# Kernel optimization log

Hardware: AMD Instinct MI355X
Metric: run time of the kernel (lower is better)

## Reference

```python
import jax, jax.numpy as jnp
import numpy as np

ALPHA = 0.25
GAMMA = 2.0
MARGIN = 1.0
LAMBDA_GRAPH = 0.1
N = 8192
D = 128


def setup_inputs() -> dict:
    key = jax.random.key(0)
    k1, k2, k3, k4 = jax.random.split(key, 4)
    preds = jax.random.normal(k1, (N,), dtype=jnp.float32)
    targets = jax.random.randint(k2, (N,), 0, 2).astype(jnp.float32)  # binary labels
    features = jax.random.normal(k3, (N, D), dtype=jnp.float32)
    graph_features = jax.random.normal(k4, (N, D), dtype=jnp.float32)
    return {"preds": preds, "targets": targets, "features": features,
            "graph_features": graph_features}


def _focal_loss(preds, targets):
    # numerically stable BCE-with-logits, reduction='none'
    bce = jnp.maximum(preds, 0.0) - preds * targets + jnp.log1p(jnp.exp(-jnp.abs(preds)))
    pt = jnp.exp(-bce)
    return jnp.mean(ALPHA * (1.0 - pt) ** GAMMA * bce)


def _contrastive_loss(features, labels):
    # squared pairwise distances via ||a||^2 + ||b||^2 - 2 a.b  -> [N, N]
    sqn = jnp.sum(features * features, axis=-1)
    sq = sqn[:, None] + sqn[None, :] - 2.0 * (features @ features.T)
    sq = jnp.maximum(sq, 0.0)
    # safe sqrt (gradient-safe at 0)
    pos = sq > 0.0
    dist = jnp.where(pos, jnp.sqrt(jnp.where(pos, sq, 1.0)), 0.0)
    same = labels[:, None] == labels[None, :]
    # same-label pairs: dist^2 == sq ; different: clamp(margin - dist, 0)^2
    per_pair = jnp.where(same, sq, jnp.maximum(MARGIN - dist, 0.0) ** 2)
    return jnp.mean(per_pair)  # sum / N^2


def _graph_reg_loss(graph_features):
    diff = graph_features[1:] - graph_features[:-1]
    return jnp.mean(jnp.sqrt(jnp.sum(diff * diff, axis=1)))


def reference(preds, targets, features, graph_features):
    return (_focal_loss(preds, targets)
            + _contrastive_loss(features, targets)
            + LAMBDA_GRAPH * _graph_reg_loss(graph_features))
```

## Files before the change

### kernel.cpp

```cpp
#include <hip/hip_runtime.h>
#include <hip/hip_bf16.h>


#define N_PTS 8192
#define DIM 128

typedef __bf16 bf16x8 __attribute__((ext_vector_type(8)));
typedef float f32x4 __attribute__((ext_vector_type(4)));

#define FBF_OFF   0
#define SQN_OFF   2097152
#define CPART_OFF 2129920
#define FPART_OFF 2163200
#define GPART_OFF 2163328
#define VPART_OFF 2164352
#define ASCR_OFF  2197120
#define BSCR_OFF  2721408

__global__ __launch_bounds__(256) void aux_kernel(const float* __restrict__ feat,
                                                  const float* __restrict__ preds,
                                                  const float* __restrict__ targets,
                                                  const float* __restrict__ gfeat,
                                                  __bf16* __restrict__ fbf,
                                                  __bf16* __restrict__ ascr,
                                                  __bf16* __restrict__ bscr,
                                                  float* __restrict__ sqn,
                                                  float* __restrict__ vpart,
                                                  float* __restrict__ f_part,
                                                  float* __restrict__ g_part) {
    __shared__ __align__(16) char smem[8192];
    const int bx = blockIdx.x;
    const int tid = threadIdx.x;
    const int w = tid >> 6;
    const int lane = tid & 63;

    if (bx < 512) {
        const int g = bx;
        const float4* feat4 = reinterpret_cast<const float4*>(feat);
        const float4 a = feat4[g * 512 + tid * 2];
        const float4 b = feat4[g * 512 + tid * 2 + 1];
        const int m = tid >> 4, c = tid & 15;
        union { __bf16 h[8]; uint4 u; } pk;
        pk.h[0] = (__bf16)a.x; pk.h[1] = (__bf16)a.y;
        pk.h[2] = (__bf16)a.z; pk.h[3] = (__bf16)a.w;
        pk.h[4] = (__bf16)b.x; pk.h[5] = (__bf16)b.y;
        pk.h[6] = (__bf16)b.z; pk.h[7] = (__bf16)b.w;
        *reinterpret_cast<uint4*>(smem + c * 256 + m * 16) = pk.u;
        if (c < 3) {
            union { __bf16 h[8]; uint4 u; } pa;
            pa.h[0] = (__bf16)(-2.f * a.x); pa.h[1] = (__bf16)(-2.f * a.y);
            pa.h[2] = (__bf16)(-2.f * a.z); pa.h[3] = (__bf16)(-2.f * a.w);
            pa.h[4] = (__bf16)(-2.f * b.x); pa.h[5] = (__bf16)(-2.f * b.y);
            pa.h[6] = (__bf16)(-2.f * b.z); pa.h[7] = (__bf16)(-2.f * b.w);
            *reinterpret_cast<uint4*>(smem + 4096 + c * 256 + m * 16) = pa.u;
            *reinterpret_cast<uint4*>(smem + 5120 + c * 256 + m * 16) = pk.u;
        }
        const float s = a.x * a.x + a.y * a.y + a.z * a.z + a.w * a.w
                      + b.x * b.x + b.y * b.y + b.z * b.z + b.w * b.w;
        reinterpret_cast<float*>(smem + 6144)[m * 16 + c] = s;
        __syncthreads();
        if (c == 3) {
            const float* S = reinterpret_cast<const float*>(smem + 6144);
            const float sq24 = S[m * 16] + S[m * 16 + 1] + S[m * 16 + 2];
            union { __bf16 h[8]; uint4 u; } pa, pb;
            #pragma unroll
            for (int k = 0; k < 8; ++k) { pa.h[k] = (__bf16)0.f; pb.h[k] = (__bf16)0.f; }
            pa.h[0] = (__bf16)sq24; pa.h[1] = (__bf16)1.f;
            pb.h[0] = (__bf16)1.f;  pb.h[1] = (__bf16)sq24;
            *reinterpret_cast<uint4*>(smem + 4096 + 3 * 256 + m * 16) = pa.u;
            *reinterpret_cast<uint4*>(smem + 5120 + 3 * 256 + m * 16) = pb.u;
        }
        if (c == 0) {
            const float* S = reinterpret_cast<const float*>(smem + 6144);
            float t = 0.f;
            #pragma unroll
            for (int k = 0; k < 16; ++k) t += S[m * 16 + k];
            sqn[g * 16 + m] = t;
        }
        __syncthreads();
        reinterpret_cast<uint4*>(fbf)[g * 256 + tid] =
            *reinterpret_cast<const uint4*>(smem + tid * 16);
        if (tid < 64)
            reinterpret_cast<uint4*>(ascr)[g * 64 + tid] =
                *reinterpret_cast<const uint4*>(smem + 4096 + tid * 16);
        else if (tid < 128)
            reinterpret_cast<uint4*>(bscr)[g * 64 + (tid - 64)] =
                *reinterpret_cast<const uint4*>(smem + 5120 + (tid - 64) * 16);
    } else if (bx < 544) {
        const int b = bx - 512;
        const float2* feat2 = reinterpret_cast<const float2*>(feat);
        float2 accA = {0.f, 0.f}, acc1 = {0.f, 0.f};
        int r = b * 256 + w * 64;
        #pragma unroll 4
        for (int i = 0; i < 64; ++i, ++r) {
            const float2 v = feat2[r * 64 + lane];
            const float tr = targets[r];
            accA.x += v.x; accA.y += v.y;
            acc1.x += tr * v.x; acc1.y += tr * v.y;
        }
        float* fA = reinterpret_cast<float*>(smem);
        float* f1 = reinterpret_cast<float*>(smem + 2048);
        fA[w * 128 + 2 * lane] = accA.x; fA[w * 128 + 2 * lane + 1] = accA.y;
        f1[w * 128 + 2 * lane] = acc1.x; f1[w * 128 + 2 * lane + 1] = acc1.y;
        __syncthreads();
        if (tid < 128) {
            const int d = tid;
            const float c1 = f1[d] + f1[128 + d] + f1[256 + d] + f1[384 + d];
            const float ca = fA[d] + fA[128 + d] + fA[256 + d] + fA[384 + d];
            vpart[b * 256 + tid] = ca - c1;
        } else {
            const int d = tid - 128;
            vpart[b * 256 + tid] = f1[d] + f1[128 + d] + f1[256 + d] + f1[384 + d];
        }
    } else if (bx < 576) {
        const int b = bx - 544;
        const int i = b * 256 + tid;
        const float p = preds[i], t = targets[i];
        const float bce = fmaxf(p, 0.f) - p * t + log1pf(expf(-fabsf(p)));
        const float pt = expf(-bce);
        const float om = 1.f - pt;
        float v = 0.25f * om * om * bce;
        #pragma unroll
        for (int off = 32; off > 0; off >>= 1) v += __shfl_down(v, off);
        float* red = reinterpret_cast<float*>(smem);
        if (lane == 0) red[w] = v;
        __syncthreads();
        if (tid == 0) f_part[b] = red[0] + red[1] + red[2] + red[3];
    } else {
        const int b = bx - 576;
        float acc = 0.f;
        #pragma unroll
        for (int it = 0; it < 8; ++it) {
            const int r = b * 4 + w + it * 1024;
            if (r < N_PTS - 1) {
                const float2 a = *reinterpret_cast<const float2*>(gfeat + r * DIM + lane * 2);
                const float2 bb = *reinterpret_cast<const float2*>(gfeat + (r + 1) * DIM + lane * 2);
                const float dx = bb.x - a.x, dy = bb.y - a.y;
                float s = dx * dx + dy * dy;
                #pragma unroll
                for (int off = 32; off > 0; off >>= 1) s += __shfl_down(s, off);
                if (lane == 0) acc += sqrtf(s);
            }
        }
        float* red = reinterpret_cast<float*>(smem);
        if (lane == 0) red[w] = acc;
        __syncthreads();
        if (tid == 0) g_part[b] = red[0] + red[1] + red[2] + red[3];
    }
}

template<bool DIAG>
__device__ __forceinline__ float scan_slow(const f32x4 (&acc)[4][4],
                                           const f32x4 (&sqni)[4], const f32x4 (&ti4)[4],
                                           const float (&sqnj)[4], const float (&tj4)[4],
                                           int wm, int wn, int quad, int m15) {
    float lsum = 0.f;
    #pragma unroll
    for (int tm = 0; tm < 4; ++tm) {
        #pragma unroll
        for (int tn = 0; tn < 4; ++tn) {
            const int jl = wn * 64 + tn * 16 + m15;
            #pragma unroll
            for (int e = 0; e < 4; ++e) {
                const float sq = sqni[tm][e] + sqnj[tn] - 2.f * acc[tm][tn][e];
                bool excl = (ti4[tm][e] == tj4[tn]);
                if (DIAG) {
                    const int il = wm * 64 + tm * 16 + quad * 4 + e;
                    excl = excl || (jl <= il);
                }
                if (!excl && sq < 1.f) {
                    const float d = sqrtf(fmaxf(sq, 0.f));
                    const float m = 1.f - d;
                    lsum += 2.f * m * m;
                }
            }
        }
    }
    return lsum;
}

__global__ __launch_bounds__(256, 4) void pair_kernel(const __bf16* __restrict__ fbf,
                                                      const __bf16* __restrict__ ascr,
                                                      const __bf16* __restrict__ bscr,
                                                      const float* __restrict__ sqn,
                                                      const float* __restrict__ targets,
                                                      float* __restrict__ c_part) {
    const int u = blockIdx.x;
    const int v = 2079 - u;
    int k = (int)((sqrtf(8.f * (float)v + 1.f) - 1.f) * 0.5f);
    while ((k + 1) * (k + 2) / 2 <= v) ++k;
    while (k * (k + 1) / 2 > v) --k;
    const int bi = 63 - k;
    const int bj = 63 - (v - k * (k + 1) / 2);

    const int tid = threadIdx.x;
    const int lane = tid & 63;
    const int wv = tid >> 6;
    const int quad = lane >> 4;
    const int m15 = lane & 15;
    const int wm = wv >> 1, wn = wv & 1;
    const int ibase = bi * 128, jbase = bj * 128;

    const uint4* aS = reinterpret_cast<const uint4*>(ascr);
    const uint4* bS = reinterpret_cast<const uint4*>(bscr);
    const int gA = bi * 8 + wm * 4, gB = bj * 8 + wn * 4;
    bf16x8 afs[4], bfs[4];
    #pragma unroll
    for (int t = 0; t < 4; ++t) {
        afs[t] = *reinterpret_cast<const bf16x8*>(aS + (gA + t) * 64 + quad * 16 + m15);
        bfs[t] = *reinterpret_cast<const bf16x8*>(bS + (gB + t) * 64 + quad * 16 + m15);
    }
    f32x4 acc[4][4];
    #pragma unroll
    for (int a = 0; a < 4; ++a)
        #pragma unroll
        for (int b = 0; b < 4; ++b) acc[a][b] = (f32x4){0.f, 0.f, 0.f, 0.f};
    #pragma unroll
    for (int tm = 0; tm < 4; ++tm)
        #pragma unroll
        for (int tn = 0; tn < 4; ++tn)
            acc[tm][tn] = __builtin_amdgcn_mfma_f32_16x16x32_bf16(
                afs[tm], bfs[tn], acc[tm][tn], 0, 0, 0);

    float minl = 1e30f;
    #pragma unroll
    for (int tm = 0; tm < 4; ++tm)
        #pragma unroll
        for (int tn = 0; tn < 4; ++tn)
            #pragma unroll
            for (int e = 0; e < 4; ++e)
                minl = fminf(minl, acc[tm][tn][e]);

    float lsum = 0.f;
    if (__any(minl < 2.f)) {
        f32x4 sqni[4], ti4[4];
        float sqnj[4], tj4[4];
        #pragma unroll
        for (int tm = 0; tm < 4; ++tm) {
            const int i0 = wm * 64 + tm * 16 + quad * 4;
            sqni[tm] = *reinterpret_cast<const f32x4*>(sqn + ibase + i0);
            ti4[tm]  = *reinterpret_cast<const f32x4*>(targets + ibase + i0);
        }
        #pragma unroll
        for (int tn = 0; tn < 4; ++tn) {
            const int jl = wn * 64 + tn * 16 + m15;
            sqnj[tn] = sqn[jbase + jl];
            tj4[tn]  = targets[jbase + jl];
        }
        #pragma unroll
        for (int a = 0; a < 4; ++a)
            #pragma unroll
            for (int b = 0; b < 4; ++b) acc[a][b] = (f32x4){0.f, 0.f, 0.f, 0.f};
        const uint4* fp = reinterpret_cast<const uint4*>(fbf);
        const uint4* base_a = fp + (bi * 8 + wm * 4) * 256 + quad * 16 + m15;
        const uint4* base_b = fp + (bj * 8 + wn * 4) * 256 + quad * 16 + m15;
        #pragma unroll
        for (int ks = 0; ks < 4; ++ks) {
            bf16x8 af[4], bfr[4];
            #pragma unroll
            for (int t = 0; t < 4; ++t) {
                af[t]  = *reinterpret_cast<const bf16x8*>(base_a + t * 256 + ks * 64);
                bfr[t] = *reinterpret_cast<const bf16x8*>(base_b + t * 256 + ks * 64);
            }
            #pragma unroll
            for (int tm = 0; tm < 4; ++tm)
                #pragma unroll
                for (int tn = 0; tn < 4; ++tn)
                    acc[tm][tn] = __builtin_amdgcn_mfma_f32_16x16x32_bf16(
                        af[tm], bfr[tn], acc[tm][tn], 0, 0, 0);
        }
        lsum = (bi == bj)
            ? scan_slow<true >(acc, sqni, ti4, sqnj, tj4, wm, wn, quad, m15)
            : scan_slow<false>(acc, sqni, ti4, sqnj, tj4, wm, wn, quad, m15);
        #pragma unroll
        for (int off = 32; off > 0; off >>= 1) lsum += __shfl_down(lsum, off);
    }
    if (lane == 0) c_part[u * 4 + wv] = lsum;
}

__global__ __launch_bounds__(256) void finalize_kernel(const float* __restrict__ c_part,
                                                       const float* __restrict__ f_part,
                                                       const float* __restrict__ g_part,
                                                       const float* __restrict__ vpart,
                                                       const float* __restrict__ sqn,
                                                       const float* __restrict__ targets,
                                                       float* __restrict__ out) {
    __shared__ float red[32];
    const int tid = threadIdx.x;
    const int w = tid >> 6, lane = tid & 63;

    float c = 0.f;
    for (int i = tid; i < 8320; i += 256) c += c_part[i];
    float f = (tid < 32) ? f_part[tid] : 0.f;
    float g = g_part[tid];

    float V = 0.f;
    #pragma unroll 8
    for (int b = 0; b < 32; ++b) V += vpart[b * 256 + tid];
    float vsq = V * V;

    float stot = 0.f, s1 = 0.f, n1 = 0.f;
    for (int i = tid; i < N_PTS; i += 256) {
        const float s = sqn[i], t = targets[i];
        stot += s; s1 += t * s; n1 += t;
    }

    #pragma unroll
    for (int off = 32; off > 0; off >>= 1) {
        c += __shfl_down(c, off);
        f += __shfl_down(f, off);
        g += __shfl_down(g, off);
        vsq  += __shfl_down(vsq, off);
        stot += __shfl_down(stot, off);
        s1   += __shfl_down(s1, off);
        n1   += __shfl_down(n1, off);
    }
    if (lane == 0) {
        red[w] = c; red[4 + w] = f; red[8 + w] = g;
        red[12 + w] = vsq; red[16 + w] = stot; red[20 + w] = s1; red[24 + w] = n1;
    }
    __syncthreads();
    if (tid == 0) {
        const double cs = (double)red[0] + red[1] + red[2] + red[3];
        const double fs = (double)red[4] + red[5] + red[6] + red[7];
        const double gs = (double)red[8] + red[9] + red[10] + red[11];
        const double v0sq = (double)red[12] + red[13];
        const double v1sq = (double)red[14] + red[15];
        const double st = (double)red[16] + red[17] + red[18] + red[19];
        const double s1s = (double)red[20] + red[21] + red[22] + red[23];
        const double n1s = (double)red[24] + red[25] + red[26] + red[27];
        const double n0s = (double)N_PTS - n1s;
        const double s0s = st - s1s;
        const double same = 2.0 * (n0s * s0s - v0sq) + 2.0 * (n1s * s1s - v1sq);
        out[0] = (float)((cs + same) / ((double)N_PTS * N_PTS)
                         + fs / N_PTS + 0.1 * (gs / (N_PTS - 1)));
    }
}

extern "C" void kernel_launch(void* const* d_in, const int* in_sizes, int n_in,
                              void* d_out, int out_size, void* d_ws, size_t ws_size,
                              hipStream_t stream) {
    const float* preds    = (const float*)d_in[0];
    const float* targets  = (const float*)d_in[1];
    const float* features = (const float*)d_in[2];
    const float* gfeat    = (const float*)d_in[3];
    char* ws = (char*)d_ws;
    __bf16* fbf   = (__bf16*)(ws + FBF_OFF);
    __bf16* ascr  = (__bf16*)(ws + ASCR_OFF);
    __bf16* bscr  = (__bf16*)(ws + BSCR_OFF);
    float* sqn    = (float*)(ws + SQN_OFF);
    float* c_part = (float*)(ws + CPART_OFF);
    float* f_part = (float*)(ws + FPART_OFF);
    float* g_part = (float*)(ws + GPART_OFF);
    float* vpart  = (float*)(ws + VPART_OFF);
    float* out = (float*)d_out;

    aux_kernel<<<832, 256, 0, stream>>>(features, preds, targets, gfeat,
                                        fbf, ascr, bscr, sqn, vpart, f_part, g_part);
    pair_kernel<<<2080, 256, 0, stream>>>(fbf, ascr, bscr, sqn, targets, c_part);
    finalize_kernel<<<1, 256, 0, stream>>>(c_part, f_part, g_part, vpart, sqn, targets, out);
}
```

Baseline: 102.4 us.

## Fuse bf16 conversion into pair kernel and replace finalize with atomic last-block reduction

Drops the bf16 pre-conversion pass and its scratch buffers. The pair blocks now load fp32 features directly, convert them to bf16 in registers and compute squared norms on the fly. The separate finalize kernel is replaced by double-precision atomic accumulators plus a block counter, so the last finishing block writes the output. The launch count drops from three to two, at the cost of redundant fp32 loads and conversions in each pair tile, plus atomic contention.

```diff
diff --git a/kernel.cpp b/kernel.cpp
--- a/kernel.cpp
+++ b/kernel.cpp
@@ -8,144 +8,82 @@
 typedef __bf16 bf16x8 __attribute__((ext_vector_type(8)));
 typedef float f32x4 __attribute__((ext_vector_type(4)));
 
-#define FBF_OFF   0
-#define SQN_OFF   2097152
-#define CPART_OFF 2129920
-#define FPART_OFF 2163200
-#define GPART_OFF 2163328
-#define VPART_OFF 2164352
-#define ASCR_OFF  2197120
-#define BSCR_OFF  2721408
-
-__global__ __launch_bounds__(256) void aux_kernel(const float* __restrict__ feat,
-                                                  const float* __restrict__ preds,
-                                                  const float* __restrict__ targets,
-                                                  const float* __restrict__ gfeat,
-                                                  __bf16* __restrict__ fbf,
-                                                  __bf16* __restrict__ ascr,
-                                                  __bf16* __restrict__ bscr,
-                                                  float* __restrict__ sqn,
-                                                  float* __restrict__ vpart,
-                                                  float* __restrict__ f_part,
-                                                  float* __restrict__ g_part) {
-    __shared__ __align__(16) char smem[8192];
-    const int bx = blockIdx.x;
+#define VPART_OFF 0
+#define SPART_OFF (128 * 256 * 4)
+#define CTRL_OFF  (SPART_OFF + 128 * 16)
+
+#define NPAIR 2080
+#define NFOCAL 32
+#define NGRAPH 256
+#define TOTAL_BLOCKS (NPAIR + NFOCAL + NGRAPH + 1)
+
+__device__ __forceinline__ bf16x8 pack8(const float4 a, const float4 b) {
+    bf16x8 r;
+    r[0] = (__bf16)a.x; r[1] = (__bf16)a.y; r[2] = (__bf16)a.z; r[3] = (__bf16)a.w;
+    r[4] = (__bf16)b.x; r[5] = (__bf16)b.y; r[6] = (__bf16)b.z; r[7] = (__bf16)b.w;
+    return r;
+}
+__device__ __forceinline__ float ssq8(const float4 a, const float4 b) {
+    return a.x * a.x + a.y * a.y + a.z * a.z + a.w * a.w
+         + b.x * b.x + b.y * b.y + b.z * b.z + b.w * b.w;
+}
+
+__global__ __launch_bounds__(256) void prep_kernel(const float* __restrict__ feat,
+                                                   const float* __restrict__ targets,
+                                                   float* __restrict__ vpart,
+                                                   float* __restrict__ spart,
+                                                   unsigned long long* __restrict__ ctrl) {
+    const int b = blockIdx.x;
     const int tid = threadIdx.x;
-    const int w = tid >> 6;
-    const int lane = tid & 63;
-
-    if (bx < 512) {
-        const int g = bx;
-        const float4* feat4 = reinterpret_cast<const float4*>(feat);
-        const float4 a = feat4[g * 512 + tid * 2];
-        const float4 b = feat4[g * 512 + tid * 2 + 1];
-        const int m = tid >> 4, c = tid & 15;
-        union { __bf16 h[8]; uint4 u; } pk;
-        pk.h[0] = (__bf16)a.x; pk.h[1] = (__bf16)a.y;
-        pk.h[2] = (__bf16)a.z; pk.h[3] = (__bf16)a.w;
-        pk.h[4] = (__bf16)b.x; pk.h[5] = (__bf16)b.y;
-        pk.h[6] = (__bf16)b.z; pk.h[7] = (__bf16)b.w;
-        *reinterpret_cast<uint4*>(smem + c * 256 + m * 16) = pk.u;
-        if (c < 3) {
-            union { __bf16 h[8]; uint4 u; } pa;
-            pa.h[0] = (__bf16)(-2.f * a.x); pa.h[1] = (__bf16)(-2.f * a.y);
-            pa.h[2] = (__bf16)(-2.f * a.z); pa.h[3] = (__bf16)(-2.f * a.w);
-            pa.h[4] = (__bf16)(-2.f * b.x); pa.h[5] = (__bf16)(-2.f * b.y);
-            pa.h[6] = (__bf16)(-2.f * b.z); pa.h[7] = (__bf16)(-2.f * b.w);
-            *reinterpret_cast<uint4*>(smem + 4096 + c * 256 + m * 16) = pa.u;
-            *reinterpret_cast<uint4*>(smem + 5120 + c * 256 + m * 16) = pk.u;
-        }
-        const float s = a.x * a.x + a.y * a.y + a.z * a.z + a.w * a.w
-                      + b.x * b.x + b.y * b.y + b.z * b.z + b.w * b.w;
-        reinterpret_cast<float*>(smem + 6144)[m * 16 + c] = s;
-        __syncthreads();
-        if (c == 3) {
-            const float* S = reinterpret_cast<const float*>(smem + 6144);
-            const float sq24 = S[m * 16] + S[m * 16 + 1] + S[m * 16 + 2];
-            union { __bf16 h[8]; uint4 u; } pa, pb;
-            #pragma unroll
-            for (int k = 0; k < 8; ++k) { pa.h[k] = (__bf16)0.f; pb.h[k] = (__bf16)0.f; }
-            pa.h[0] = (__bf16)sq24; pa.h[1] = (__bf16)1.f;
-            pb.h[0] = (__bf16)1.f;  pb.h[1] = (__bf16)sq24;
-            *reinterpret_cast<uint4*>(smem + 4096 + 3 * 256 + m * 16) = pa.u;
-            *reinterpret_cast<uint4*>(smem + 5120 + 3 * 256 + m * 16) = pb.u;
-        }
-        if (c == 0) {
-            const float* S = reinterpret_cast<const float*>(smem + 6144);
-            float t = 0.f;
-            #pragma unroll
-            for (int k = 0; k < 16; ++k) t += S[m * 16 + k];
-            sqn[g * 16 + m] = t;
-        }
-        __syncthreads();
-        reinterpret_cast<uint4*>(fbf)[g * 256 + tid] =
-            *reinterpret_cast<const uint4*>(smem + tid * 16);
-        if (tid < 64)
-            reinterpret_cast<uint4*>(ascr)[g * 64 + tid] =
-                *reinterpret_cast<const uint4*>(smem + 4096 + tid * 16);
-        else if (tid < 128)
-            reinterpret_cast<uint4*>(bscr)[g * 64 + (tid - 64)] =
-                *reinterpret_cast<const uint4*>(smem + 5120 + (tid - 64) * 16);
-    } else if (bx < 544) {
-        const int b = bx - 512;
-        const float2* feat2 = reinterpret_cast<const float2*>(feat);
-        float2 accA = {0.f, 0.f}, acc1 = {0.f, 0.f};
-        int r = b * 256 + w * 64;
-        #pragma unroll 4
-        for (int i = 0; i < 64; ++i, ++r) {
-            const float2 v = feat2[r * 64 + lane];
-            const float tr = targets[r];
-            accA.x += v.x; accA.y += v.y;
-            acc1.x += tr * v.x; acc1.y += tr * v.y;
-        }
-        float* fA = reinterpret_cast<float*>(smem);
-        float* f1 = reinterpret_cast<float*>(smem + 2048);
-        fA[w * 128 + 2 * lane] = accA.x; fA[w * 128 + 2 * lane + 1] = accA.y;
-        f1[w * 128 + 2 * lane] = acc1.x; f1[w * 128 + 2 * lane + 1] = acc1.y;
-        __syncthreads();
-        if (tid < 128) {
-            const int d = tid;
-            const float c1 = f1[d] + f1[128 + d] + f1[256 + d] + f1[384 + d];
-            const float ca = fA[d] + fA[128 + d] + fA[256 + d] + fA[384 + d];
-            vpart[b * 256 + tid] = ca - c1;
-        } else {
-            const int d = tid - 128;
-            vpart[b * 256 + tid] = f1[d] + f1[128 + d] + f1[256 + d] + f1[384 + d];
-        }
-    } else if (bx < 576) {
-        const int b = bx - 544;
-        const int i = b * 256 + tid;
-        const float p = preds[i], t = targets[i];
-        const float bce = fmaxf(p, 0.f) - p * t + log1pf(expf(-fabsf(p)));
-        const float pt = expf(-bce);
-        const float om = 1.f - pt;
-        float v = 0.25f * om * om * bce;
-        #pragma unroll
-        for (int off = 32; off > 0; off >>= 1) v += __shfl_down(v, off);
-        float* red = reinterpret_cast<float*>(smem);
-        if (lane == 0) red[w] = v;
-        __syncthreads();
-        if (tid == 0) f_part[b] = red[0] + red[1] + red[2] + red[3];
+    if (b == 128) {
+        if (tid == 0) {
+            *reinterpret_cast<unsigned*>(ctrl) = 0u;
+            double* a = reinterpret_cast<double*>(ctrl);
+            a[1] = 0.0; a[2] = 0.0; a[3] = 0.0;
+        }
+        return;
+    }
+    __shared__ float fA[512], f1[512];
+    __shared__ float sred[4][3];
+    const int w = tid >> 6, lane = tid & 63;
+    const float2* feat2 = reinterpret_cast<const float2*>(feat);
+    float2 accA = {0.f, 0.f}, acc1 = {0.f, 0.f};
+    float ssqA = 0.f, ssq1 = 0.f, n1 = 0.f;
+    int r = b * 64 + w * 16;
+    #pragma unroll 4
+    for (int i = 0; i < 16; ++i, ++r) {
+        const float2 v = feat2[r * 64 + lane];
+        const float tr = targets[r];
+        accA.x += v.x; accA.y += v.y;
+        acc1.x += tr * v.x; acc1.y += tr * v.y;
+        const float s2 = v.x * v.x + v.y * v.y;
+        ssqA += s2; ssq1 += tr * s2; n1 += tr;
+    }
+    fA[w * 128 + 2 * lane] = accA.x; fA[w * 128 + 2 * lane + 1] = accA.y;
+    f1[w * 128 + 2 * lane] = acc1.x; f1[w * 128 + 2 * lane + 1] = acc1.y;
+    #pragma unroll
+    for (int off = 32; off > 0; off >>= 1) {
+        ssqA += __shfl_down(ssqA, off);
+        ssq1 += __shfl_down(ssq1, off);
+    }
+    if (lane == 0) { sred[w][0] = ssqA; sred[w][1] = ssq1; sred[w][2] = n1; }
+    __syncthreads();
+    if (tid < 128) {
+        const int d = tid;
+        const float c1 = f1[d] + f1[128 + d] + f1[256 + d] + f1[384 + d];
+        const float ca = fA[d] + fA[128 + d] + fA[256 + d] + fA[384 + d];
+        vpart[b * 256 + tid] = ca - c1;
     } else {
-        const int b = bx - 576;
-        float acc = 0.f;
-        #pragma unroll
-        for (int it = 0; it < 8; ++it) {
-            const int r = b * 4 + w + it * 1024;
-            if (r < N_PTS - 1) {
-                const float2 a = *reinterpret_cast<const float2*>(gfeat + r * DIM + lane * 2);
-                const float2 bb = *reinterpret_cast<const float2*>(gfeat + (r + 1) * DIM + lane * 2);
-                const float dx = bb.x - a.x, dy = bb.y - a.y;
-                float s = dx * dx + dy * dy;
-                #pragma unroll
-                for (int off = 32; off > 0; off >>= 1) s += __shfl_down(s, off);
-                if (lane == 0) acc += sqrtf(s);
-            }
-        }
-        float* red = reinterpret_cast<float*>(smem);
-        if (lane == 0) red[w] = acc;
-        __syncthreads();
-        if (tid == 0) g_part[b] = red[0] + red[1] + red[2] + red[3];
+        const int d = tid - 128;
+        vpart[b * 256 + tid] = f1[d] + f1[128 + d] + f1[256 + d] + f1[384 + d];
+    }
+    if (tid == 0) {
+        float4 s;
+        s.x = sred[0][0] + sred[1][0] + sred[2][0] + sred[3][0];
+        s.y = sred[0][1] + sred[1][1] + sred[2][1] + sred[3][1];
+        s.z = sred[0][2] + sred[1][2] + sred[2][2] + sred[3][2];
+        s.w = 0.f;
+        *reinterpret_cast<float4*>(spart + b * 4) = s;
     }
 }
 
@@ -179,161 +117,220 @@
     return lsum;
 }
 
-__global__ __launch_bounds__(256, 4) void pair_kernel(const __bf16* __restrict__ fbf,
-                                                      const __bf16* __restrict__ ascr,
-                                                      const __bf16* __restrict__ bscr,
-                                                      const float* __restrict__ sqn,
+__global__ __launch_bounds__(256, 4) void main_kernel(const float* __restrict__ feat,
+                                                      const float* __restrict__ preds,
                                                       const float* __restrict__ targets,
-                                                      float* __restrict__ c_part) {
-    const int u = blockIdx.x;
-    const int v = 2079 - u;
-    int k = (int)((sqrtf(8.f * (float)v + 1.f) - 1.f) * 0.5f);
-    while ((k + 1) * (k + 2) / 2 <= v) ++k;
-    while (k * (k + 1) / 2 > v) --k;
-    const int bi = 63 - k;
-    const int bj = 63 - (v - k * (k + 1) / 2);
-
-    const int tid = threadIdx.x;
-    const int lane = tid & 63;
-    const int wv = tid >> 6;
-    const int quad = lane >> 4;
-    const int m15 = lane & 15;
-    const int wm = wv >> 1, wn = wv & 1;
-    const int ibase = bi * 128, jbase = bj * 128;
-
-    const uint4* aS = reinterpret_cast<const uint4*>(ascr);
-    const uint4* bS = reinterpret_cast<const uint4*>(bscr);
-    const int gA = bi * 8 + wm * 4, gB = bj * 8 + wn * 4;
-    bf16x8 afs[4], bfs[4];
-    #pragma unroll
-    for (int t = 0; t < 4; ++t) {
-        afs[t] = *reinterpret_cast<const bf16x8*>(aS + (gA + t) * 64 + quad * 16 + m15);
-        bfs[t] = *reinterpret_cast<const bf16x8*>(bS + (gB + t) * 64 + quad * 16 + m15);
-    }
-    f32x4 acc[4][4];
-    #pragma unroll
-    for (int a = 0; a < 4; ++a)
-        #pragma unroll
-        for (int b = 0; b < 4; ++b) acc[a][b] = (f32x4){0.f, 0.f, 0.f, 0.f};
-    #pragma unroll
-    for (int tm = 0; tm < 4; ++tm)
-        #pragma unroll
-        for (int tn = 0; tn < 4; ++tn)
-            acc[tm][tn] = __builtin_amdgcn_mfma_f32_16x16x32_bf16(
-                afs[tm], bfs[tn], acc[tm][tn], 0, 0, 0);
-
-    float minl = 1e30f;
-    #pragma unroll
-    for (int tm = 0; tm < 4; ++tm)
-        #pragma unroll
-        for (int tn = 0; tn < 4; ++tn)
-            #pragma unroll
-            for (int e = 0; e < 4; ++e)
-                minl = fminf(minl, acc[tm][tn][e]);
-
-    float lsum = 0.f;
-    if (__any(minl < 2.f)) {
-        f32x4 sqni[4], ti4[4];
-        float sqnj[4], tj4[4];
-        #pragma unroll
-        for (int tm = 0; tm < 4; ++tm) {
-            const int i0 = wm * 64 + tm * 16 + quad * 4;
-            sqni[tm] = *reinterpret_cast<const f32x4*>(sqn + ibase + i0);
-            ti4[tm]  = *reinterpret_cast<const f32x4*>(targets + ibase + i0);
-        }
-        #pragma unroll
-        for (int tn = 0; tn < 4; ++tn) {
-            const int jl = wn * 64 + tn * 16 + m15;
-            sqnj[tn] = sqn[jbase + jl];
-            tj4[tn]  = targets[jbase + jl];
-        }
-        #pragma unroll
-        for (int a = 0; a < 4; ++a)
-            #pragma unroll
-            for (int b = 0; b < 4; ++b) acc[a][b] = (f32x4){0.f, 0.f, 0.f, 0.f};
-        const uint4* fp = reinterpret_cast<const uint4*>(fbf);
-        const uint4* base_a = fp + (bi * 8 + wm * 4) * 256 + quad * 16 + m15;
-        const uint4* base_b = fp + (bj * 8 + wn * 4) * 256 + quad * 16 + m15;
-        #pragma unroll
-        for (int ks = 0; ks < 4; ++ks) {
-            bf16x8 af[4], bfr[4];
-            #pragma unroll
-            for (int t = 0; t < 4; ++t) {
-                af[t]  = *reinterpret_cast<const bf16x8*>(base_a + t * 256 + ks * 64);
-                bfr[t] = *reinterpret_cast<const bf16x8*>(base_b + t * 256 + ks * 64);
-            }
-            #pragma unroll
-            for (int tm = 0; tm < 4; ++tm)
-                #pragma unroll
-                for (int tn = 0; tn < 4; ++tn)
-                    acc[tm][tn] = __builtin_amdgcn_mfma_f32_16x16x32_bf16(
-                        af[tm], bfr[tn], acc[tm][tn], 0, 0, 0);
-        }
-        lsum = (bi == bj)
-            ? scan_slow<true >(acc, sqni, ti4, sqnj, tj4, wm, wn, quad, m15)
-            : scan_slow<false>(acc, sqni, ti4, sqnj, tj4, wm, wn, quad, m15);
-        #pragma unroll
-        for (int off = 32; off > 0; off >>= 1) lsum += __shfl_down(lsum, off);
-    }
-    if (lane == 0) c_part[u * 4 + wv] = lsum;
-}
-
-__global__ __launch_bounds__(256) void finalize_kernel(const float* __restrict__ c_part,
-                                                       const float* __restrict__ f_part,
-                                                       const float* __restrict__ g_part,
-                                                       const float* __restrict__ vpart,
-                                                       const float* __restrict__ sqn,
-                                                       const float* __restrict__ targets,
-                                                       float* __restrict__ out) {
-    __shared__ float red[32];
+                                                      const float* __restrict__ gfeat,
+                                                      const float* __restrict__ vpart,
+                                                      const float* __restrict__ spart,
+                                                      unsigned* __restrict__ counter,
+                                                      double* __restrict__ accs,
+                                                      float* __restrict__ out) {
+    __shared__ __align__(16) float smem[1024];
+    const int bx = blockIdx.x;
     const int tid = threadIdx.x;
     const int w = tid >> 6, lane = tid & 63;
-
-    float c = 0.f;
-    for (int i = tid; i < 8320; i += 256) c += c_part[i];
-    float f = (tid < 32) ? f_part[tid] : 0.f;
-    float g = g_part[tid];
-
-    float V = 0.f;
-    #pragma unroll 8
-    for (int b = 0; b < 32; ++b) V += vpart[b * 256 + tid];
-    float vsq = V * V;
-
-    float stot = 0.f, s1 = 0.f, n1 = 0.f;
-    for (int i = tid; i < N_PTS; i += 256) {
-        const float s = sqn[i], t = targets[i];
-        stot += s; s1 += t * s; n1 += t;
-    }
-
-    #pragma unroll
-    for (int off = 32; off > 0; off >>= 1) {
-        c += __shfl_down(c, off);
-        f += __shfl_down(f, off);
-        g += __shfl_down(g, off);
-        vsq  += __shfl_down(vsq, off);
-        stot += __shfl_down(stot, off);
-        s1   += __shfl_down(s1, off);
-        n1   += __shfl_down(n1, off);
-    }
-    if (lane == 0) {
-        red[w] = c; red[4 + w] = f; red[8 + w] = g;
-        red[12 + w] = vsq; red[16 + w] = stot; red[20 + w] = s1; red[24 + w] = n1;
-    }
-    __syncthreads();
+    double addv = 0.0;
+    int acc_idx = 1;
+
+    if (bx < NPAIR) {
+        const int u = bx;
+        const int vv = 2079 - u;
+        int k = (int)((sqrtf(8.f * (float)vv + 1.f) - 1.f) * 0.5f);
+        while ((k + 1) * (k + 2) / 2 <= vv) ++k;
+        while (k * (k + 1) / 2 > vv) --k;
+        const int bi = 63 - k;
+        const int bj = 63 - (vv - k * (k + 1) / 2);
+
+        const int quad = lane >> 4, m15 = lane & 15;
+        const int wm = w >> 1, wn = w & 1;
+        const int ibase = bi * 128 + wm * 64, jbase = bj * 128 + wn * 64;
+
+        bf16x8 afs[4], bfs[4];
+        float sA[4], sB[4];
+        #pragma unroll
+        for (int t = 0; t < 4; ++t) {
+            const float* pa = feat + (ibase + t * 16 + m15) * DIM + 8 * quad;
+            const float4 a0 = *reinterpret_cast<const float4*>(pa);
+            const float4 a1 = *reinterpret_cast<const float4*>(pa + 4);
+            afs[t] = pack8(a0, a1);
+            float s = ssq8(a0, a1);
+            s += __shfl_xor(s, 16); s += __shfl_xor(s, 32);
+            sA[t] = s;
+            const float* pb = feat + (jbase + t * 16 + m15) * DIM + 8 * quad;
+            const float4 b0 = *reinterpret_cast<const float4*>(pb);
+            const float4 b1 = *reinterpret_cast<const float4*>(pb + 4);
+            bfs[t] = pack8(b0, b1);
+            float sb = ssq8(b0, b1);
+            sb += __shfl_xor(sb, 16); sb += __shfl_xor(sb, 32);
+            sB[t] = sb;
+        }
+        f32x4 acc[4][4];
+        #pragma unroll
+        for (int a = 0; a < 4; ++a)
+            #pragma unroll
+            for (int b = 0; b < 4; ++b) acc[a][b] = (f32x4){0.f, 0.f, 0.f, 0.f};
+        #pragma unroll
+        for (int tm = 0; tm < 4; ++tm)
+            #pragma unroll
+            for (int tn = 0; tn < 4; ++tn)
+                acc[tm][tn] = __builtin_amdgcn_mfma_f32_16x16x32_bf16(
+                    afs[tm], bfs[tn], acc[tm][tn], 0, 0, 0);
+
+        float minv = 1e30f;
+        #pragma unroll
+        for (int tm = 0; tm < 4; ++tm) {
+            #pragma unroll
+            for (int e = 0; e < 4; ++e) {
+                const float sa = __shfl(sA[tm], quad * 4 + e);
+                #pragma unroll
+                for (int tn = 0; tn < 4; ++tn)
+                    minv = fminf(minv, sa + sB[tn] - 2.f * acc[tm][tn][e]);
+            }
+        }
+
+        float lsum = 0.f;
+        if (__any(minv < 2.f)) {
+            float qi = 0.f, qj = 0.f;
+            {
+                const float4* ri = reinterpret_cast<const float4*>(feat + (ibase + lane) * DIM);
+                const float4* rj = reinterpret_cast<const float4*>(feat + (jbase + lane) * DIM);
+                #pragma unroll 8
+                for (int c2 = 0; c2 < 32; ++c2) {
+                    const float4 x = ri[c2]; qi += x.x * x.x + x.y * x.y + x.z * x.z + x.w * x.w;
+                    const float4 y = rj[c2]; qj += y.x * y.x + y.y * y.y + y.z * y.z + y.w * y.w;
+                }
+            }
+            f32x4 sqni[4], ti4[4];
+            float sqnj[4], tj4[4];
+            #pragma unroll
+            for (int tm = 0; tm < 4; ++tm) {
+                #pragma unroll
+                for (int e = 0; e < 4; ++e) sqni[tm][e] = __shfl(qi, tm * 16 + quad * 4 + e);
+                ti4[tm] = *reinterpret_cast<const f32x4*>(targets + ibase + tm * 16 + quad * 4);
+            }
+            #pragma unroll
+            for (int tn = 0; tn < 4; ++tn) {
+                sqnj[tn] = __shfl(qj, tn * 16 + m15);
+                tj4[tn] = targets[jbase + tn * 16 + m15];
+            }
+            for (int ks = 1; ks < 4; ++ks) {
+                bf16x8 af2[4], bf2[4];
+                #pragma unroll
+                for (int t = 0; t < 4; ++t) {
+                    const float* pa = feat + (ibase + t * 16 + m15) * DIM + 8 * (quad + 4 * ks);
+                    af2[t] = pack8(*reinterpret_cast<const float4*>(pa),
+                                   *reinterpret_cast<const float4*>(pa + 4));
+                    const float* pb = feat + (jbase + t * 16 + m15) * DIM + 8 * (quad + 4 * ks);
+                    bf2[t] = pack8(*reinterpret_cast<const float4*>(pb),
+                                   *reinterpret_cast<const float4*>(pb + 4));
+                }
+                #pragma unroll
+                for (int tm = 0; tm < 4; ++tm)
+                    #pragma unroll
+                    for (int tn = 0; tn < 4; ++tn)
+                        acc[tm][tn] = __builtin_amdgcn_mfma_f32_16x16x32_bf16(
+                            af2[tm], bf2[tn], acc[tm][tn], 0, 0, 0);
+            }
+            lsum = (bi == bj)
+                ? scan_slow<true >(acc, sqni, ti4, sqnj, tj4, wm, wn, quad, m15)
+                : scan_slow<false>(acc, sqni, ti4, sqnj, tj4, wm, wn, quad, m15);
+            #pragma unroll
+            for (int off = 32; off > 0; off >>= 1) lsum += __shfl_down(lsum, off);
+        }
+        if (lane == 0) smem[w] = lsum;
+        __syncthreads();
+        if (tid == 0) {
+            addv = (double)(smem[0] + smem[1] + smem[2] + smem[3]);
+            acc_idx = 1;
+        }
+    } else if (bx < NPAIR + NFOCAL) {
+        const int b = bx - NPAIR;
+        const int i = b * 256 + tid;
+        const float p = preds[i], t = targets[i];
+        const float bce = fmaxf(p, 0.f) - p * t + log1pf(expf(-fabsf(p)));
+        const float pt = expf(-bce);
+        const float om = 1.f - pt;
+        float fv = 0.25f * om * om * bce;
+        #pragma unroll
+        for (int off = 32; off > 0; off >>= 1) fv += __shfl_down(fv, off);
+        if (lane == 0) smem[w] = fv;
+        __syncthreads();
+        if (tid == 0) {
+            addv = (double)(smem[0] + smem[1] + smem[2] + smem[3]);
+            acc_idx = 2;
+        }
+    } else if (bx < NPAIR + NFOCAL + NGRAPH) {
+        const int b = bx - NPAIR - NFOCAL;
+        float ga = 0.f;
+        #pragma unroll
+        for (int it = 0; it < 8; ++it) {
+            const int r = b * 4 + w + it * 1024;
+            if (r < N_PTS - 1) {
+                const float2 a = *reinterpret_cast<const float2*>(gfeat + r * DIM + lane * 2);
+                const float2 bb = *reinterpret_cast<const float2*>(gfeat + (r + 1) * DIM + lane * 2);
+                const float dx = bb.x - a.x, dy = bb.y - a.y;
+                float s = dx * dx + dy * dy;
+                #pragma unroll
+                for (int off = 32; off > 0; off >>= 1) s += __shfl_down(s, off);
+                if (lane == 0) ga += sqrtf(s);
+            }
+        }
+        if (lane == 0) smem[w] = ga;
+        __syncthreads();
+        if (tid == 0) {
+            addv = (double)(smem[0] + smem[1] + smem[2] + smem[3]);
+            acc_idx = 3;
+        }
+    } else {
+        float V = 0.f;
+        #pragma unroll 8
+        for (int b2 = 0; b2 < 128; ++b2) V += vpart[b2 * 256 + tid];
+        double vsq = (double)V * (double)V;
+        #pragma unroll
+        for (int off = 32; off > 0; off >>= 1) vsq += __shfl_down(vsq, off);
+        double* dred = reinterpret_cast<double*>(smem);
+        if (lane == 0) dred[w] = vsq;
+        double st = 0.0, s1 = 0.0, n1 = 0.0;
+        if (tid < 128) {
+            const float4 s = *reinterpret_cast<const float4*>(spart + tid * 4);
+            st = s.x; s1 = s.y; n1 = s.z;
+        }
+        #pragma unroll
+        for (int off = 32; off > 0; off >>= 1) {
+            st += __shfl_down(st, off);
+            s1 += __shfl_down(s1, off);
+            n1 += __shfl_down(n1, off);
+        }
+        if (lane == 0) { dred[4 + w * 3] = st; dred[5 + w * 3] = s1; dred[6 + w * 3] = n1; }
+        __syncthreads();
+        if (tid == 0) {
+            const double v0sq = dred[0] + dred[1];
+            const double v1sq = dred[2] + dred[3];
+            const double stot = dred[4] + dred[7];
+            const double s1s  = dred[5] + dred[8];
+            const double n1s  = dred[6] + dred[9];
+            const double n0s = (double)N_PTS - n1s;
+            const double s0s = stot - s1s;
+            addv = 2.0 * (n0s * s0s - v0sq) + 2.0 * (n1s * s1s - v1sq);
+            acc_idx = 1;
+        }
+    }
+
     if (tid == 0) {
-        const double cs = (double)red[0] + red[1] + red[2] + red[3];
-        const double fs = (double)red[4] + red[5] + red[6] + red[7];
-        const double gs = (double)red[8] + red[9] + red[10] + red[11];
-        const double v0sq = (double)red[12] + red[13];
-        const double v1sq = (double)red[14] + red[15];
-        const double st = (double)red[16] + red[17] + red[18] + red[19];
-        const double s1s = (double)red[20] + red[21] + red[22] + red[23];
-        const double n1s = (double)red[24] + red[25] + red[26] + red[27];
-        const double n0s = (double)N_PTS - n1s;
-        const double s0s = st - s1s;
-        const double same = 2.0 * (n0s * s0s - v0sq) + 2.0 * (n1s * s1s - v1sq);
-        out[0] = (float)((cs + same) / ((double)N_PTS * N_PTS)
-                         + fs / N_PTS + 0.1 * (gs / (N_PTS - 1)));
+        if (addv != 0.0) {
+            atomicAdd(accs + acc_idx, addv);
+            asm volatile("s_waitcnt vmcnt(0)" ::: "memory");
+        }
+        const unsigned old = atomicAdd(counter, 1u);
+        if (old == TOTAL_BLOCKS - 1) {
+            const double c = atomicAdd(accs + 1, 0.0);
+            const double f = atomicAdd(accs + 2, 0.0);
+            const double g = atomicAdd(accs + 3, 0.0);
+            out[0] = (float)(c / ((double)N_PTS * (double)N_PTS)
+                             + f / (double)N_PTS
+                             + 0.1 * (g / (double)(N_PTS - 1)));
+        }
     }
 }
 
@@ -345,18 +342,13 @@
     const float* features = (const float*)d_in[2];
     const float* gfeat    = (const float*)d_in[3];
     char* ws = (char*)d_ws;
-    __bf16* fbf   = (__bf16*)(ws + FBF_OFF);
-    __bf16* ascr  = (__bf16*)(ws + ASCR_OFF);
-    __bf16* bscr  = (__bf16*)(ws + BSCR_OFF);
-    float* sqn    = (float*)(ws + SQN_OFF);
-    float* c_part = (float*)(ws + CPART_OFF);
-    float* f_part = (float*)(ws + FPART_OFF);
-    float* g_part = (float*)(ws + GPART_OFF);
-    float* vpart  = (float*)(ws + VPART_OFF);
-    float* out = (float*)d_out;
-
-    aux_kernel<<<832, 256, 0, stream>>>(features, preds, targets, gfeat,
-                                        fbf, ascr, bscr, sqn, vpart, f_part, g_part);
-    pair_kernel<<<2080, 256, 0, stream>>>(fbf, ascr, bscr, sqn, targets, c_part);
-    finalize_kernel<<<1, 256, 0, stream>>>(c_part, f_part, g_part, vpart, sqn, targets, out);
-}
+    float* vpart = (float*)(ws + VPART_OFF);
+    float* spart = (float*)(ws + SPART_OFF);
+    unsigned long long* ctrl = (unsigned long long*)(ws + CTRL_OFF);
+
+    prep_kernel<<<129, 256, 0, stream>>>(features, targets, vpart, spart, ctrl);
+    main_kernel<<<TOTAL_BLOCKS, 256, 0, stream>>>(features, preds, targets, gfeat,
+                                                  vpart, spart,
+                                                  (unsigned*)ctrl, (double*)ctrl,
+                                                  (float*)d_out);
+}
```

New measurement: 121.5 us. 1.19x slower.
